# Kernel tuning notes

Measured on AMD Instinct MI355X. Metric: run time of the kernel, lower is better.

## Reference

```python
import jax, jax.numpy as jnp
import numpy as np

INPUT_DIM = 16
HIDDEN_DIM = 2048
OUTPUT_DIM = 3
SEQ_LEN = 8192


def setup_inputs() -> dict:
    key = jax.random.key(0)
    ks = jax.random.split(key, 9)
    s = 1.0 / np.sqrt(HIDDEN_DIM)  # PyTorch LSTMCell/Linear init scale
    return {
        "state_action": jax.random.normal(ks[0], (SEQ_LEN, INPUT_DIM), dtype=jnp.float32),
        "W_ih": jax.random.uniform(ks[1], (4 * HIDDEN_DIM, INPUT_DIM), jnp.float32, -s, s),
        "W_hh": jax.random.uniform(ks[2], (4 * HIDDEN_DIM, HIDDEN_DIM), jnp.float32, -s, s),
        "b_ih": jax.random.uniform(ks[3], (4 * HIDDEN_DIM,), jnp.float32, -s, s),
        "b_hh": jax.random.uniform(ks[4], (4 * HIDDEN_DIM,), jnp.float32, -s, s),
        "W_uvw": jax.random.uniform(ks[5], (OUTPUT_DIM, HIDDEN_DIM), jnp.float32, -s, s),
        "b_uvw": jax.random.uniform(ks[6], (OUTPUT_DIM,), jnp.float32, -s, s),
        "W_pqr": jax.random.uniform(ks[7], (OUTPUT_DIM, HIDDEN_DIM), jnp.float32, -s, s),
        "b_pqr": jax.random.uniform(ks[8], (OUTPUT_DIM,), jnp.float32, -s, s),
    }


def reference(state_action, W_ih, W_hh, b_ih, b_hh, W_uvw, b_uvw, W_pqr, b_pqr):
    hd = W_hh.shape[1]
    # Precompute input projections for all timesteps: [H, 4*hd]
    x_proj = state_action @ W_ih.T + b_ih + b_hh

    def step(carry, xp):
        h, c = carry  # each [hd]
        gates = xp + h @ W_hh.T  # [4*hd]
        i, f, g, o = jnp.split(gates, 4)  # PyTorch gate order: input, forget, cell, output
        i = jax.nn.sigmoid(i)
        f = jax.nn.sigmoid(f)
        g = jnp.tanh(g)
        o = jax.nn.sigmoid(o)
        c_new = f * c + i * g
        h_new = o * jnp.tanh(c_new)
        return (h_new, c_new), h_new

    init = (jnp.zeros((hd,), jnp.float32), jnp.zeros((hd,), jnp.float32))
    _, hs = jax.lax.scan(step, init, x_proj)  # hs: [H, hd]

    uvw = hs @ W_uvw.T + b_uvw  # [H, 3]
    pqr = hs @ W_pqr.T + b_pqr  # [H, 3]
    # Original returns a list of [1, 6]; stacked+squeezed form is [H, 6]
    return jnp.concatenate([uvw, pqr], axis=-1)
```

## Files before the change

kernel.cpp:

```cpp
#include <hip/hip_runtime.h>
#include <cstdint>
#include <cstddef>

#define SEQ   8192
#define HD    2048
#define IND   16
#define NBLK  256
#define NTHR  256
#define NSLOT 1024
#define NXCD  8

#define GATE_TICKS 24ull
#define TIGHT_TRIES 4

typedef _Float16 h2  __attribute__((ext_vector_type(2)));
typedef unsigned u32x4 __attribute__((ext_vector_type(4)));

union paircvt { h2 v; unsigned u; };

__device__ __forceinline__ float fdot2f(h2 a, h2 b, float c) {
#if defined(__has_builtin)
#if __has_builtin(__builtin_amdgcn_fdot2)
    return __builtin_amdgcn_fdot2(a, b, c, false);
#else
    return c + (float)a.x * (float)b.x + (float)a.y * (float)b.y;
#endif
#else
    return c + (float)a.x * (float)b.x + (float)a.y * (float)b.y;
#endif
}

__device__ __forceinline__ float sigmoid_f(float x) {
    return 1.f / (1.f + __expf(-x));
}
__device__ __forceinline__ float tanh_f(float x) {
    float e = __expf(2.f * x);
    return 1.f - 2.f / (e + 1.f);
}

__device__ __forceinline__ unsigned my_xcd() {
    unsigned x;
    asm volatile("s_getreg_b32 %0, hwreg(HW_REG_XCC_ID, 0, 4)" : "=s"(x));
    return x & (NXCD - 1);
}

__device__ __forceinline__ float dpp_xor1(float x) {
    int i = __builtin_bit_cast(int, x);
    int r = __builtin_amdgcn_mov_dpp(i, 0xB1, 0xf, 0xf, false);
    return __builtin_bit_cast(float, r);
}
__device__ __forceinline__ float dpp_xor2(float x) {
    int i = __builtin_bit_cast(int, x);
    int r = __builtin_amdgcn_mov_dpp(i, 0x4E, 0xf, 0xf, false);
    return __builtin_bit_cast(float, r);
}
__device__ __forceinline__ float xor16_add(float x) {
    float a = x, b = x;
    asm volatile("v_permlane16_swap_b32 %0, %1" : "+v"(a), "+v"(b));
    return a + b;
}
__device__ __forceinline__ float xor32_add(float x) {
    float a = x, b = x;
    asm volatile("v_permlane32_swap_b32 %0, %1" : "+v"(a), "+v"(b));
    return a + b;
}

__global__ __launch_bounds__(NTHR, 1) void lstm_persist(
    const float* __restrict__ sa,
    const float* __restrict__ W_ih,
    const float* __restrict__ W_hh,
    const float* __restrict__ b_ih,
    const float* __restrict__ b_hh,
    unsigned long long* __restrict__ hrep,
    _Float16* __restrict__ hs16)
{
    const int b   = blockIdx.x;
    const int tid = threadIdx.x;
    const int w   = tid >> 6;
    const int L   = tid & 63;
    const unsigned xcd = my_xcd();

    __shared__ h2 hh2[16 * 64];

    const int ubase = b * 8 + 2 * w;

    h2 wreg[8][16];
#pragma unroll
    for (int r = 0; r < 8; ++r) {
        const int row = (r & 3) * HD + ubase + (r >> 2);
        const float4* Wr = (const float4*)(W_hh + (size_t)row * HD + L * 32);
#pragma unroll
        for (int q = 0; q < 8; ++q) {
            float4 f = Wr[q];
            h2 lo; lo.x = (_Float16)f.x; lo.y = (_Float16)f.y;
            h2 hi; hi.x = (_Float16)f.z; hi.y = (_Float16)f.w;
            wreg[r][2 * q]     = lo;
            wreg[r][2 * q + 1] = hi;
        }
    }
    const int rowL = (L & 3) * HD + ubase + ((L >> 2) & 1);
    float wih[IND];
    {
        const float4* Wi = (const float4*)(W_ih + (size_t)rowL * IND);
#pragma unroll
        for (int q = 0; q < 4; ++q) {
            float4 f = Wi[q];
            wih[4 * q]     = f.x;
            wih[4 * q + 1] = f.y;
            wih[4 * q + 2] = f.z;
            wih[4 * q + 3] = f.w;
        }
    }
    const float bias = b_ih[rowL] + b_hh[rowL];

    h2* wp0; h2* wp1; h2* wp2; h2* wp3;
    {
        const int pa = 2 * tid, pb = 2 * tid + 1;
        const int pc = 512 + 2 * tid, pd = 513 + 2 * tid;
        wp0 = &hh2[(pa & 15) * 64 + (((pa >> 4) ^ (2 * (pa & 15))) & 63)];
        wp1 = &hh2[(pb & 15) * 64 + (((pb >> 4) ^ (2 * (pb & 15))) & 63)];
        wp2 = &hh2[(pc & 15) * 64 + (((pc >> 4) ^ (2 * (pc & 15))) & 63)];
        wp3 = &hh2[(pd & 15) * 64 + (((pd >> 4) ^ (2 * (pd & 15))) & 63)];
    }
    const h2* rp[16];
#pragma unroll
    for (int k = 0; k < 16; ++k)
        rp[k] = &hh2[k * 64 + ((L ^ (2 * k)) & 63)];

    float sat[IND];
    {
        const float4* s4 = (const float4*)(sa);
#pragma unroll
        for (int q = 0; q < 4; ++q) {
            float4 f = s4[q];
            sat[4 * q]     = f.x;
            sat[4 * q + 1] = f.y;
            sat[4 * q + 2] = f.z;
            sat[4 * q + 3] = f.w;
        }
    }

    float c = 0.f;
    unsigned long long pubclk = 0;

    for (unsigned t = 0; t < SEQ; ++t) {
        float xp = bias;
#pragma unroll
        for (int k = 0; k < IND; ++k) xp += sat[k] * wih[k];

        if (t + 1 < SEQ) {
            const float4* s4 = (const float4*)(sa + (size_t)(t + 1) * IND);
#pragma unroll
            for (int q = 0; q < 4; ++q) {
                float4 f = s4[q];
                sat[4 * q]     = f.x;
                sat[4 * q + 1] = f.y;
                sat[4 * q + 2] = f.z;
                sat[4 * q + 3] = f.w;
            }
        }

        if (t) {
            unsigned long long now;
            do {
                now = __builtin_amdgcn_s_memrealtime();
            } while (now - pubclk < GATE_TICKS);
        }

        const unsigned pin = t & 1;
        const uint32_t* base =
            (const uint32_t*)(hrep + ((size_t)xcd * 2 + pin) * NSLOT);
        const uint32_t* pp0 = base + 4 * tid;
        const uint32_t* pp1 = base + 1024 + 4 * tid;
        u32x4 m0, m1;
        int tries = 0;
        for (;;) {
            asm volatile(
                "global_load_dwordx4 %0, %2, off sc1\n\t"
                "global_load_dwordx4 %1, %3, off sc1\n\t"
                "s_waitcnt vmcnt(0)"
                : "=v"(m0), "=v"(m1)
                : "v"(pp0), "v"(pp1) : "memory");
            bool ok = (m0.y == t) & (m0.w == t) & (m1.y == t) & (m1.w == t);
            if (ok) break;
            if (++tries > TIGHT_TRIES) __builtin_amdgcn_s_sleep(1);
        }

        {
            paircvt cv;
            cv.u = m0.x; *wp0 = cv.v;
            cv.u = m0.z; *wp1 = cv.v;
            cv.u = m1.x; *wp2 = cv.v;
            cv.u = m1.z; *wp3 = cv.v;
        }
        __syncthreads();

        h2 hv[16];
#pragma unroll
        for (int k = 0; k < 16; ++k)
            hv[k] = *rp[k];

        float p[8] = {0.f, 0.f, 0.f, 0.f, 0.f, 0.f, 0.f, 0.f};
#pragma unroll
        for (int r = 0; r < 8; ++r)
#pragma unroll
            for (int k = 0; k < 16; ++k)
                p[r] = fdot2f(wreg[r][k], hv[k], p[r]);

        const bool h1 = (L & 1), h2b = (L & 2), h4 = (L & 4);
        float v0, v1, v2, v3;
        {
            float k0 = h1 ? p[1] : p[0], s0 = h1 ? p[0] : p[1];
            v0 = k0 + dpp_xor1(s0);
            float k1 = h1 ? p[3] : p[2], s1 = h1 ? p[2] : p[3];
            v1 = k1 + dpp_xor1(s1);
            float k2 = h1 ? p[5] : p[4], s2 = h1 ? p[4] : p[5];
            v2 = k2 + dpp_xor1(s2);
            float k3 = h1 ? p[7] : p[6], s3 = h1 ? p[6] : p[7];
            v3 = k3 + dpp_xor1(s3);
        }
        float w0, w1;
        {
            float k0 = h2b ? v1 : v0, s0 = h2b ? v0 : v1;
            w0 = k0 + dpp_xor2(s0);
            float k1 = h2b ? v3 : v2, s1 = h2b ? v2 : v3;
            w1 = k1 + dpp_xor2(s1);
        }
        float tot;
        {
            float k0 = h4 ? w1 : w0, s0 = h4 ? w0 : w1;
            tot = k0 + __shfl_xor(s0, 4, 64);
        }
        tot += __shfl_xor(tot, 8, 64);
        tot = xor16_add(tot);
        tot = xor32_add(tot);
        tot += xp;

        const int ub4 = L & 4;
        float gi = __shfl(tot, ub4 + 0, 8);
        float gf = __shfl(tot, ub4 + 1, 8);
        float gg = __shfl(tot, ub4 + 2, 8);
        float go = __shfl(tot, ub4 + 3, 8);
        float ii = sigmoid_f(gi);
        float ff = sigmoid_f(gf);
        float g  = tanh_f(gg);
        float oo = sigmoid_f(go);
        c = ff * c + ii * g;
        float h = oo * tanh_f(c);

        {
            float hA = __shfl(h, 0, 8);
            float hB = __shfl(h, 4, 8);
            paircvt pk;
            pk.v.x = (_Float16)hA;
            pk.v.y = (_Float16)hB;
            const unsigned pout = (t + 1) & 1;
            const size_t slot = (size_t)b * 4 + w;
            unsigned long long msg =
                ((unsigned long long)(t + 1) << 32) | (unsigned long long)pk.u;
            if (L < 8)
                __hip_atomic_store(
                    &hrep[((size_t)L * 2 + pout) * NSLOT + slot], msg,
                    __ATOMIC_RELAXED, __HIP_MEMORY_SCOPE_AGENT);
            if (L == 8)
                ((unsigned*)hs16)[(size_t)t * (HD / 2) + b * 4 + w] = pk.u;
        }
        pubclk = __builtin_amdgcn_s_memrealtime();
    }
}

__global__ __launch_bounds__(256) void out_proj_kernel(
    const _Float16* __restrict__ hs16,
    const float* __restrict__ W_uvw, const float* __restrict__ b_uvw,
    const float* __restrict__ W_pqr, const float* __restrict__ b_pqr,
    float* __restrict__ out)
{
    __shared__ float Ws[6 * HD];
    const int tid = threadIdx.x;
    for (int i = tid; i < 3 * HD; i += 256) Ws[i] = W_uvw[i];
    for (int i = tid; i < 3 * HD; i += 256) Ws[3 * HD + i] = W_pqr[i];
    __syncthreads();

    const int w = tid >> 6, L = tid & 63;
#pragma unroll
    for (int r = 0; r < 4; ++r) {
        const int t = blockIdx.x * 16 + w * 4 + r;
        const _Float16* hrow = hs16 + (size_t)t * HD;
        float acc[6] = {0.f, 0.f, 0.f, 0.f, 0.f, 0.f};
        for (int cidx = L; cidx < HD; cidx += 64) {
            float hval = (float)hrow[cidx];
#pragma unroll
            for (int j = 0; j < 6; ++j) acc[j] += hval * Ws[j * HD + cidx];
        }
#pragma unroll
        for (int j = 0; j < 6; ++j) {
#pragma unroll
            for (int d = 1; d < 64; d <<= 1)
                acc[j] += __shfl_xor(acc[j], d, 64);
        }
        if (L == 0) {
#pragma unroll
            for (int j = 0; j < 6; ++j)
                out[(size_t)t * 6 + j] =
                    acc[j] + (j < 3 ? b_uvw[j] : b_pqr[j - 3]);
        }
    }
}

extern "C" void kernel_launch(void* const* d_in, const int* in_sizes, int n_in,
                              void* d_out, int out_size, void* d_ws, size_t ws_size,
                              hipStream_t stream) {
    (void)in_sizes; (void)n_in; (void)out_size; (void)ws_size;

    const float* sa    = (const float*)d_in[0];
    const float* W_ih  = (const float*)d_in[1];
    const float* W_hh  = (const float*)d_in[2];
    const float* b_ih  = (const float*)d_in[3];
    const float* b_hh  = (const float*)d_in[4];
    const float* W_uvw = (const float*)d_in[5];
    const float* b_uvw = (const float*)d_in[6];
    const float* W_pqr = (const float*)d_in[7];
    const float* b_pqr = (const float*)d_in[8];
    float* out = (float*)d_out;

    char* ws = (char*)d_ws;
    _Float16* hs16 = (_Float16*)ws;
    unsigned long long* hrep =
        (unsigned long long*)(ws + (size_t)SEQ * HD * 2);

    hipMemsetAsync(hrep, 0, (size_t)NXCD * 2 * NSLOT * 8, stream);

    hipLaunchKernelGGL(lstm_persist, dim3(NBLK), dim3(NTHR), 0, stream,
                       sa, W_ih, W_hh, b_ih, b_hh, hrep, hs16);
    hipLaunchKernelGGL(out_proj_kernel, dim3(SEQ / 16), dim3(256), 0, stream,
                       hs16, W_uvw, b_uvw, W_pqr, b_pqr, out);
}
```

Measured before the change: 14.31 ms.

## Have each wave poll the full hidden vector directly, dropping LDS exchange and block barrier

```diff
diff --git a/kernel.cpp b/kernel.cpp
--- a/kernel.cpp
+++ b/kernel.cpp
@@ -10,8 +10,8 @@
 #define NSLOT 1024
 #define NXCD  8
 
-#define GATE_TICKS 24ull
-#define TIGHT_TRIES 4
+#define GATE_TICKS 16ull
+#define TIGHT_TRIES 8
 
 typedef _Float16 h2  __attribute__((ext_vector_type(2)));
 typedef unsigned u32x4 __attribute__((ext_vector_type(4)));
@@ -80,8 +80,6 @@
     const int L   = tid & 63;
     const unsigned xcd = my_xcd();
 
-    __shared__ h2 hh2[16 * 64];
-
     const int ubase = b * 8 + 2 * w;
 
     h2 wreg[8][16];
@@ -113,19 +111,8 @@
     }
     const float bias = b_ih[rowL] + b_hh[rowL];
 
-    h2* wp0; h2* wp1; h2* wp2; h2* wp3;
-    {
-        const int pa = 2 * tid, pb = 2 * tid + 1;
-        const int pc = 512 + 2 * tid, pd = 513 + 2 * tid;
-        wp0 = &hh2[(pa & 15) * 64 + (((pa >> 4) ^ (2 * (pa & 15))) & 63)];
-        wp1 = &hh2[(pb & 15) * 64 + (((pb >> 4) ^ (2 * (pb & 15))) & 63)];
-        wp2 = &hh2[(pc & 15) * 64 + (((pc >> 4) ^ (2 * (pc & 15))) & 63)];
-        wp3 = &hh2[(pd & 15) * 64 + (((pd >> 4) ^ (2 * (pd & 15))) & 63)];
-    }
-    const h2* rp[16];
-#pragma unroll
-    for (int k = 0; k < 16; ++k)
-        rp[k] = &hh2[k * 64 + ((L ^ (2 * k)) & 63)];
+    const int slot = b * 4 + w;
+    const int ppos = ((slot & 15) >> 1) * 128 + 2 * (slot >> 4) + (slot & 1);
 
     float sat[IND];
     {
@@ -142,6 +129,9 @@
 
     float c = 0.f;
     unsigned long long pubclk = 0;
+
+    const unsigned voff0 = (unsigned)(L * 16);
+    const unsigned voff1 = (unsigned)(L * 16 + 4096);
 
     for (unsigned t = 0; t < SEQ; ++t) {
         float xp = bias;
@@ -168,37 +158,45 @@
         }
 
         const unsigned pin = t & 1;
-        const uint32_t* base =
-            (const uint32_t*)(hrep + ((size_t)xcd * 2 + pin) * NSLOT);
-        const uint32_t* pp0 = base + 4 * tid;
-        const uint32_t* pp1 = base + 1024 + 4 * tid;
-        u32x4 m0, m1;
+        const unsigned long long baseaddr =
+            (unsigned long long)(hrep + ((size_t)xcd * 2 + pin) * NSLOT);
+        u32x4 m0, m1, m2, m3, m4, m5, m6, m7;
         int tries = 0;
         for (;;) {
             asm volatile(
-                "global_load_dwordx4 %0, %2, off sc1\n\t"
-                "global_load_dwordx4 %1, %3, off sc1\n\t"
+                "global_load_dwordx4 %0, %8, %10 sc1\n\t"
+                "global_load_dwordx4 %1, %8, %10 offset:1024 sc1\n\t"
+                "global_load_dwordx4 %2, %8, %10 offset:2048 sc1\n\t"
+                "global_load_dwordx4 %3, %8, %10 offset:3072 sc1\n\t"
+                "global_load_dwordx4 %4, %9, %10 sc1\n\t"
+                "global_load_dwordx4 %5, %9, %10 offset:1024 sc1\n\t"
+                "global_load_dwordx4 %6, %9, %10 offset:2048 sc1\n\t"
+                "global_load_dwordx4 %7, %9, %10 offset:3072 sc1\n\t"
                 "s_waitcnt vmcnt(0)"
-                : "=v"(m0), "=v"(m1)
-                : "v"(pp0), "v"(pp1) : "memory");
-            bool ok = (m0.y == t) & (m0.w == t) & (m1.y == t) & (m1.w == t);
-            if (ok) break;
+                : "=v"(m0), "=v"(m1), "=v"(m2), "=v"(m3),
+                  "=v"(m4), "=v"(m5), "=v"(m6), "=v"(m7)
+                : "v"(voff0), "v"(voff1), "s"(baseaddr)
+                : "memory");
+            bool ok = (m0.y == t) & (m0.w == t) & (m1.y == t) & (m1.w == t)
+                    & (m2.y == t) & (m2.w == t) & (m3.y == t) & (m3.w == t)
+                    & (m4.y == t) & (m4.w == t) & (m5.y == t) & (m5.w == t)
+                    & (m6.y == t) & (m6.w == t) & (m7.y == t) & (m7.w == t);
+            if (__all(ok)) break;
             if (++tries > TIGHT_TRIES) __builtin_amdgcn_s_sleep(1);
         }
 
+        h2 hv[16];
         {
             paircvt cv;
-            cv.u = m0.x; *wp0 = cv.v;
-            cv.u = m0.z; *wp1 = cv.v;
-            cv.u = m1.x; *wp2 = cv.v;
-            cv.u = m1.z; *wp3 = cv.v;
-        }
-        __syncthreads();
-
-        h2 hv[16];
-#pragma unroll
-        for (int k = 0; k < 16; ++k)
-            hv[k] = *rp[k];
+            cv.u = m0.x; hv[0]  = cv.v;  cv.u = m0.z; hv[1]  = cv.v;
+            cv.u = m1.x; hv[2]  = cv.v;  cv.u = m1.z; hv[3]  = cv.v;
+            cv.u = m2.x; hv[4]  = cv.v;  cv.u = m2.z; hv[5]  = cv.v;
+            cv.u = m3.x; hv[6]  = cv.v;  cv.u = m3.z; hv[7]  = cv.v;
+            cv.u = m4.x; hv[8]  = cv.v;  cv.u = m4.z; hv[9]  = cv.v;
+            cv.u = m5.x; hv[10] = cv.v;  cv.u = m5.z; hv[11] = cv.v;
+            cv.u = m6.x; hv[12] = cv.v;  cv.u = m6.z; hv[13] = cv.v;
+            cv.u = m7.x; hv[14] = cv.v;  cv.u = m7.z; hv[15] = cv.v;
+        }
 
         float p[8] = {0.f, 0.f, 0.f, 0.f, 0.f, 0.f, 0.f, 0.f};
 #pragma unroll
@@ -255,15 +253,14 @@
             pk.v.x = (_Float16)hA;
             pk.v.y = (_Float16)hB;
             const unsigned pout = (t + 1) & 1;
-            const size_t slot = (size_t)b * 4 + w;
             unsigned long long msg =
                 ((unsigned long long)(t + 1) << 32) | (unsigned long long)pk.u;
             if (L < 8)
                 __hip_atomic_store(
-                    &hrep[((size_t)L * 2 + pout) * NSLOT + slot], msg,
+                    &hrep[((size_t)L * 2 + pout) * NSLOT + ppos], msg,
                     __ATOMIC_RELAXED, __HIP_MEMORY_SCOPE_AGENT);
             if (L == 8)
-                ((unsigned*)hs16)[(size_t)t * (HD / 2) + b * 4 + w] = pk.u;
+                ((unsigned*)hs16)[(size_t)t * (HD / 2) + slot] = pk.u;
         }
         pubclk = __builtin_amdgcn_s_memrealtime();
     }
```

Measured after the change: 15.57 ms. +8.8%, slower.
